# Performance work log

Hardware: AMD Instinct MI355X
Metric: run time of the kernel (lower is better)

Reference implementation:

```python
import jax, jax.numpy as jnp
import numpy as np

HIDDEN = 1024
EXPAND = 2
D_REC = HIDDEN * EXPAND
INTER = 4096
B, T = 4, 4096


def _rmsnorm(x, w, eps=1e-6):
    var = jnp.mean(x * x, axis=-1, keepdims=True)
    return x * jax.lax.rsqrt(var + eps) * w


def setup_inputs() -> dict:
    key = jax.random.key(0)
    ks = jax.random.split(key, 11)
    s = lambda fan: 1.0 / np.sqrt(fan)
    return {
        "x": jax.random.normal(ks[0], (B, T, HIDDEN), dtype=jnp.float32),
        "ln1_w": jnp.ones((HIDDEN,), dtype=jnp.float32),
        "ln2_w": jnp.ones((HIDDEN,), dtype=jnp.float32),
        "w_in": jax.random.normal(ks[1], (D_REC, HIDDEN), dtype=jnp.float32) * s(HIDDEN),
        "w_gate": jax.random.normal(ks[2], (D_REC, HIDDEN), dtype=jnp.float32) * s(HIDDEN),
        "a_param": jax.random.normal(ks[3], (D_REC,), dtype=jnp.float32) * 0.1,
        "w_a": jax.random.normal(ks[4], (D_REC, D_REC), dtype=jnp.float32) * s(D_REC),
        "w_out": jax.random.normal(ks[5], (HIDDEN, D_REC), dtype=jnp.float32) * s(D_REC),
        "w_mlp_gate": jax.random.normal(ks[6], (INTER, HIDDEN), dtype=jnp.float32) * s(HIDDEN),
        "w_mlp_up": jax.random.normal(ks[7], (INTER, HIDDEN), dtype=jnp.float32) * s(HIDDEN),
        "w_mlp_down": jax.random.normal(ks[8], (HIDDEN, INTER), dtype=jnp.float32) * s(INTER),
    }


def _hawk_scan(x_in, a):
    # x_in, a: [B, T, D_REC]; h_t = a_t*h_{t-1} + sqrt(1-a_t^2+eps)*x_t
    xs = jnp.moveaxis(x_in, 1, 0)  # [T, B, D]
    As = jnp.moveaxis(a, 1, 0)

    def step(state, inp):
        a_t, x_t = inp
        new = a_t * state + jnp.sqrt(1.0 - a_t * a_t + 1e-8) * x_t
        return new, new

    init = jnp.zeros(x_in.shape[::2], dtype=x_in.dtype)  # [B, D]
    _, ys = jax.lax.scan(step, init, (As, xs))
    return jnp.moveaxis(ys, 0, 1)  # [B, T, D]


def reference(x, ln1_w, ln2_w, w_in, w_gate, a_param, w_a, w_out,
              w_mlp_gate, w_mlp_up, w_mlp_down):
    h = _rmsnorm(x, ln1_w)
    x_in = h @ w_in.T                     # [B,T,D_REC]
    gate = jax.nn.sigmoid(h @ w_gate.T)
    a = jax.nn.sigmoid(a_param + x_in @ w_a.T)
    y = gate * _hawk_scan(x_in, a)
    x = x + y @ w_out.T
    h2 = _rmsnorm(x, ln2_w)
    mlp = (jax.nn.silu(h2 @ w_mlp_gate.T) * (h2 @ w_mlp_up.T)) @ w_mlp_down.T
    return x + mlp
```

## Files before the change

kernel.cpp:

```cpp
#include <hip/hip_runtime.h>
#include <cstdint>
#include <cmath>


typedef unsigned short u16;
typedef _Float16 f16;
typedef __bf16 bf16x8 __attribute__((ext_vector_type(8)));
typedef float  f32x4  __attribute__((ext_vector_type(4)));

#define BM 128
#define BN 128
#define BK 64

#define HID   1024
#define DREC  2048
#define INTER 4096
#define BT    16384
#define TLEN  4096
#define NCHAN 8192
#define CHUNK 256
#define NCH   16

__device__ __forceinline__ float b2f(u16 u) {
  union { unsigned int i; float f; } v; v.i = ((unsigned int)u) << 16; return v.f;
}
__device__ __forceinline__ u16 f2bf(float f) {
  unsigned int u = __builtin_bit_cast(unsigned int, f);
  u += 0x7FFFu + ((u >> 16) & 1u);
  return (u16)(u >> 16);
}
__device__ __forceinline__ float sigm(float x) { return 1.f / (1.f + expf(-x)); }

typedef __attribute__((address_space(1))) void as1_void;
typedef __attribute__((address_space(3))) void as3_void;
__device__ __forceinline__ void async16(const void* g, void* l) {
  __builtin_amdgcn_global_load_lds((as1_void*)g, (as3_void*)l, 16, 0, 0);
}

__global__ void f2b_kernel(const float* __restrict__ in, u16* __restrict__ out, int n4) {
  int i = blockIdx.x * 256 + threadIdx.x;
  if (i < n4) {
    float4 v = ((const float4*)in)[i];
    ushort4 o;
    o.x = f2bf(v.x); o.y = f2bf(v.y); o.z = f2bf(v.z); o.w = f2bf(v.w);
    ((ushort4*)out)[i] = o;
  }
}

__global__ void rmsnorm_kernel(const float* __restrict__ x, const float* __restrict__ w,
                               u16* __restrict__ out) {
  const int row = blockIdx.x;
  const int tid = threadIdx.x;
  float4 v = ((const float4*)(x + (size_t)row * HID))[tid];
  float ss = v.x * v.x + v.y * v.y + v.z * v.z + v.w * v.w;
#pragma unroll
  for (int o = 32; o > 0; o >>= 1) ss += __shfl_down(ss, o);
  __shared__ float red[4];
  const int lane = tid & 63, wv = tid >> 6;
  if (lane == 0) red[wv] = ss;
  __syncthreads();
  float tot = red[0] + red[1] + red[2] + red[3];
  float sc = rsqrtf(tot * (1.f / (float)HID) + 1e-6f);
  float4 wv4 = ((const float4*)w)[tid];
  ushort4 o;
  o.x = f2bf(v.x * sc * wv4.x); o.y = f2bf(v.y * sc * wv4.y);
  o.z = f2bf(v.z * sc * wv4.z); o.w = f2bf(v.w * sc * wv4.w);
  ((ushort4*)(out + (size_t)row * HID))[tid] = o;
}

enum { EPI_LOGIT = 0, EPI_ADDF = 1 };

template <int EPI>
__global__ __launch_bounds__(256, 2)
void gemm1(const u16* __restrict__ A, const u16* __restrict__ W,
           int K, int N, int ldA, int ldW,
           float* outf, f16* outz, const float* auxf) {
  __shared__ alignas(16) u16 sA[BM * BK];
  __shared__ alignas(16) u16 sB[BN * BK];

  const int tid  = threadIdx.x;
  const int lane = tid & 63;
  const int wv   = tid >> 6;
  const int wm   = wv & 1;
  const int wn   = wv >> 1;
  const int lm   = lane & 15;
  const int quad = lane >> 4;

  const int row0 = blockIdx.x * BM;
  const int col0 = blockIdx.y * BN;

  f32x4 acc[4][4];
#pragma unroll
  for (int i = 0; i < 4; ++i)
#pragma unroll
    for (int j = 0; j < 4; ++j) acc[i][j] = (f32x4)0.f;

  for (int k0 = 0; k0 < K; k0 += BK) {
#pragma unroll
    for (int i = 0; i < 4; ++i) {
      int p = i * 256 + tid;
      int r = p >> 3;
      int sg = (p & 7) ^ (r & 7);
      async16(A + (size_t)(row0 + r) * ldA + (k0 + sg * 8), (char*)sA + p * 16);
    }
#pragma unroll
    for (int i = 0; i < 4; ++i) {
      int p = i * 256 + tid;
      int r = p >> 3;
      int sg = (p & 7) ^ (r & 7);
      async16(W + (size_t)(col0 + r) * ldW + (k0 + sg * 8), (char*)sB + p * 16);
    }
    __syncthreads();

#pragma unroll
    for (int h = 0; h < 2; ++h) {
      bf16x8 af[4], bf[4];
#pragma unroll
      for (int mi = 0; mi < 4; ++mi) {
        int r = wm * 64 + mi * 16 + lm;
        af[mi] = ((const bf16x8*)sA)[r * 8 + ((h * 4 + quad) ^ (r & 7))];
      }
#pragma unroll
      for (int ni = 0; ni < 4; ++ni) {
        int c = wn * 64 + ni * 16 + lm;
        bf[ni] = ((const bf16x8*)sB)[c * 8 + ((h * 4 + quad) ^ (c & 7))];
      }
#pragma unroll
      for (int mi = 0; mi < 4; ++mi)
#pragma unroll
        for (int ni = 0; ni < 4; ++ni)
          acc[mi][ni] = __builtin_amdgcn_mfma_f32_16x16x32_bf16(af[mi], bf[ni], acc[mi][ni], 0, 0, 0);
    }
    __syncthreads();
  }

#pragma unroll
  for (int mi = 0; mi < 4; ++mi) {
    const int rbase = row0 + wm * 64 + mi * 16 + quad * 4;
#pragma unroll
    for (int ni = 0; ni < 4; ++ni) {
      const int cg = col0 + wn * 64 + ni * 16 + lm;
      f32x4 v = acc[mi][ni];
#pragma unroll
      for (int rr = 0; rr < 4; ++rr) {
        size_t idx = (size_t)(rbase + rr) * N + cg;
        float t = v[rr];
        if constexpr (EPI == EPI_LOGIT) {
          outz[idx] = (f16)(t + auxf[cg]);
        } else {
          outf[idx] = t + auxf[idx];
        }
      }
    }
  }
}

enum { EPI2_XG = 0, EPI2_SM = 1 };

template <int EPI>
__global__ __launch_bounds__(256, 2)
void gemm2(const u16* __restrict__ A, const u16* __restrict__ W0,
           const u16* __restrict__ W1,
           int K, int N, int ldA, int ldW,
           u16* out0, u16* out1) {
  __shared__ alignas(16) u16 sA[BM * BK];
  __shared__ alignas(16) u16 sB0[BN * BK];
  __shared__ alignas(16) u16 sB1[BN * BK];

  const int tid  = threadIdx.x;
  const int lane = tid & 63;
  const int wv   = tid >> 6;
  const int wm   = wv & 1;
  const int wn   = wv >> 1;
  const int lm   = lane & 15;
  const int quad = lane >> 4;

  const int row0 = blockIdx.x * BM;
  const int col0 = blockIdx.y * BN;

  f32x4 acc0[4][4], acc1[4][4];
#pragma unroll
  for (int i = 0; i < 4; ++i)
#pragma unroll
    for (int j = 0; j < 4; ++j) { acc0[i][j] = (f32x4)0.f; acc1[i][j] = (f32x4)0.f; }

  for (int k0 = 0; k0 < K; k0 += BK) {
#pragma unroll
    for (int i = 0; i < 4; ++i) {
      int p = i * 256 + tid;
      int r = p >> 3;
      int sg = (p & 7) ^ (r & 7);
      size_t go = (size_t)(col0 + r) * ldW + (k0 + sg * 8);
      async16(A + (size_t)(row0 + r) * ldA + (k0 + sg * 8), (char*)sA + p * 16);
      async16(W0 + go, (char*)sB0 + p * 16);
      async16(W1 + go, (char*)sB1 + p * 16);
    }
    __syncthreads();

#pragma unroll
    for (int h = 0; h < 2; ++h) {
      bf16x8 af[4], b0[4], b1[4];
#pragma unroll
      for (int mi = 0; mi < 4; ++mi) {
        int r = wm * 64 + mi * 16 + lm;
        af[mi] = ((const bf16x8*)sA)[r * 8 + ((h * 4 + quad) ^ (r & 7))];
      }
#pragma unroll
      for (int ni = 0; ni < 4; ++ni) {
        int c = wn * 64 + ni * 16 + lm;
        int o = c * 8 + ((h * 4 + quad) ^ (c & 7));
        b0[ni] = ((const bf16x8*)sB0)[o];
        b1[ni] = ((const bf16x8*)sB1)[o];
      }
#pragma unroll
      for (int mi = 0; mi < 4; ++mi)
#pragma unroll
        for (int ni = 0; ni < 4; ++ni) {
          acc0[mi][ni] = __builtin_amdgcn_mfma_f32_16x16x32_bf16(af[mi], b0[ni], acc0[mi][ni], 0, 0, 0);
          acc1[mi][ni] = __builtin_amdgcn_mfma_f32_16x16x32_bf16(af[mi], b1[ni], acc1[mi][ni], 0, 0, 0);
        }
    }
    __syncthreads();
  }

#pragma unroll
  for (int mi = 0; mi < 4; ++mi) {
    const int rbase = row0 + wm * 64 + mi * 16 + quad * 4;
#pragma unroll
    for (int ni = 0; ni < 4; ++ni) {
      const int cg = col0 + wn * 64 + ni * 16 + lm;
#pragma unroll
      for (int rr = 0; rr < 4; ++rr) {
        size_t idx = (size_t)(rbase + rr) * N + cg;
        float v0 = acc0[mi][ni][rr];
        float v1 = acc1[mi][ni][rr];
        if constexpr (EPI == EPI2_XG) {
          out0[idx] = f2bf(v0);
          out1[idx] = f2bf(sigm(v1));
        } else {
          out0[idx] = f2bf(v0 * sigm(v0) * v1);
        }
      }
    }
  }
}

__global__ void scan_phase1(const f16* __restrict__ z, const u16* __restrict__ xin,
                            float* __restrict__ ch_h, float* __restrict__ ch_p) {
  int gtid = blockIdx.x * 256 + threadIdx.x;
  int c = gtid >> 13;
  int chan = gtid & (NCHAN - 1);
  int b = chan >> 11;
  int d = chan & (DREC - 1);
  size_t base = ((size_t)b * TLEN + (size_t)c * CHUNK) * DREC + d;
  float h = 0.f, P = 1.f;
#pragma unroll 8
  for (int t = 0; t < CHUNK; ++t) {
    size_t i = base + (size_t)t * DREC;
    float at = sigm((float)z[i]);
    float xt = b2f(xin[i]);
    h = at * h + sqrtf(1.f - at * at + 1e-8f) * xt;
    P *= at;
  }
  ch_h[gtid] = h;
  ch_p[gtid] = P;
}

__global__ void scan_phase2(float* __restrict__ ch_h, const float* __restrict__ ch_p) {
  int chan = blockIdx.x * 256 + threadIdx.x;
  float H = 0.f;
#pragma unroll
  for (int c = 0; c < NCH; ++c) {
    int i = c * NCHAN + chan;
    float he = ch_h[i];
    float P  = ch_p[i];
    ch_h[i] = H;
    H = he + P * H;
  }
}

__global__ void scan_phase3(const f16* __restrict__ z, const u16* __restrict__ xin,
                            u16* gate_y, const float* __restrict__ ch_h) {
  int gtid = blockIdx.x * 256 + threadIdx.x;
  int c = gtid >> 13;
  int chan = gtid & (NCHAN - 1);
  int b = chan >> 11;
  int d = chan & (DREC - 1);
  size_t base = ((size_t)b * TLEN + (size_t)c * CHUNK) * DREC + d;
  float h = ch_h[gtid];
#pragma unroll 8
  for (int t = 0; t < CHUNK; ++t) {
    size_t i = base + (size_t)t * DREC;
    float at = sigm((float)z[i]);
    float xt = b2f(xin[i]);
    h = at * h + sqrtf(1.f - at * at + 1e-8f) * xt;
    gate_y[i] = f2bf(b2f(gate_y[i]) * h);
  }
}

extern "C" void kernel_launch(void* const* d_in, const int* in_sizes, int n_in,
                              void* d_out, int out_size, void* d_ws, size_t ws_size,
                              hipStream_t stream) {
  const float* x      = (const float*)d_in[0];
  const float* ln1    = (const float*)d_in[1];
  const float* ln2    = (const float*)d_in[2];
  const float* w_in   = (const float*)d_in[3];
  const float* w_gate = (const float*)d_in[4];
  const float* a_par  = (const float*)d_in[5];
  const float* w_a    = (const float*)d_in[6];
  const float* w_out  = (const float*)d_in[7];
  const float* w_mg   = (const float*)d_in[8];
  const float* w_mu   = (const float*)d_in[9];
  const float* w_md   = (const float*)d_in[10];
  float* out = (float*)d_out;
  char* ws = (char*)d_ws;

  const size_t MB = 1024ull * 1024ull;
  u16* wb_in  = (u16*)(ws + 0 * MB);
  u16* wb_gt  = (u16*)(ws + 4 * MB);
  u16* wb_a   = (u16*)(ws + 8 * MB);
  u16* wb_out = (u16*)(ws + 16 * MB);
  u16* wb_mg  = (u16*)(ws + 20 * MB);
  u16* wb_mu  = (u16*)(ws + 28 * MB);
  u16* wb_md  = (u16*)(ws + 36 * MB);
  u16* hbuf  = (u16*)(ws + 44 * MB);
  f16* zbuf  = (f16*)(ws + 44 * MB);
  u16* gateb = (u16*)(ws + 108 * MB);
  u16* mbuf  = (u16*)(ws + 108 * MB);
  float* chh = (float*)(ws + 172 * MB);
  float* chp = (float*)(ws + 172 * MB + 512 * 1024);
  u16* xinb = (u16*)d_out;

  f2b_kernel<<<2048, 256, 0, stream>>>(w_in,   wb_in,  DREC * HID / 4);
  f2b_kernel<<<2048, 256, 0, stream>>>(w_gate, wb_gt,  DREC * HID / 4);
  f2b_kernel<<<4096, 256, 0, stream>>>(w_a,    wb_a,   DREC * DREC / 4);
  f2b_kernel<<<2048, 256, 0, stream>>>(w_out,  wb_out, HID * DREC / 4);
  f2b_kernel<<<4096, 256, 0, stream>>>(w_mg,   wb_mg,  INTER * HID / 4);
  f2b_kernel<<<4096, 256, 0, stream>>>(w_mu,   wb_mu,  INTER * HID / 4);
  f2b_kernel<<<4096, 256, 0, stream>>>(w_md,   wb_md,  HID * INTER / 4);

  rmsnorm_kernel<<<BT, 256, 0, stream>>>(x, ln1, hbuf);

  gemm2<EPI2_XG><<<dim3(BT / BM, DREC / BN), 256, 0, stream>>>(
      hbuf, wb_in, wb_gt, HID, DREC, HID, HID, xinb, gateb);

  gemm1<EPI_LOGIT><<<dim3(BT / BM, DREC / BN), 256, 0, stream>>>(
      xinb, wb_a, DREC, DREC, DREC, DREC, nullptr, zbuf, a_par);

  scan_phase1<<<512, 256, 0, stream>>>(zbuf, xinb, chh, chp);
  scan_phase2<<<NCHAN / 256, 256, 0, stream>>>(chh, chp);
  scan_phase3<<<512, 256, 0, stream>>>(zbuf, xinb, gateb, chh);

  gemm1<EPI_ADDF><<<dim3(BT / BM, HID / BN), 256, 0, stream>>>(
      gateb, wb_out, DREC, HID, DREC, DREC, out, nullptr, x);

  rmsnorm_kernel<<<BT, 256, 0, stream>>>(out, ln2, hbuf);

  for (int half = 0; half < 2; ++half) {
    const u16* wmg_h = wb_mg + (size_t)half * 2048 * HID;
    const u16* wmu_h = wb_mu + (size_t)half * 2048 * HID;
    const u16* wmd_h = wb_md + (size_t)half * 2048;
    gemm2<EPI2_SM><<<dim3(BT / BM, 2048 / BN), 256, 0, stream>>>(
        hbuf, wmg_h, wmu_h, HID, 2048, HID, HID, mbuf, nullptr);
    gemm1<EPI_ADDF><<<dim3(BT / BM, HID / BN), 256, 0, stream>>>(
        mbuf, wmd_h, 2048, HID, 2048, INTER, out, nullptr, out);
  }
}
```

Before: 1.273 ms.

## Shrink dual-GEMM N tile, raise occupancy, pair scan channels, fuse weight casts

The dual-output GEMM now uses 64-wide N tiles with half the accumulators, and both GEMM kernels request 3 blocks per CU instead of 2, to cut register and LDS pressure and raise occupancy. The scan kernels each process two adjacent channels with 32-bit vector loads and stores, halving thread count and widening memory transactions. The seven weight-conversion launches are merged into one kernel to reduce launch overhead. Smaller tiles reload the A tile more often, and the tighter register budget from launch_bounds 3 may cause spills in gemm1.

```diff
diff --git a/kernel.cpp b/kernel.cpp
--- a/kernel.cpp
+++ b/kernel.cpp
@@ -20,6 +20,7 @@
 #define NCHAN 8192
 #define CHUNK 256
 #define NCH   16
+#define NPAIR 4096
 
 __device__ __forceinline__ float b2f(u16 u) {
   union { unsigned int i; float f; } v; v.i = ((unsigned int)u) << 16; return v.f;
@@ -37,14 +38,25 @@
   __builtin_amdgcn_global_load_lds((as1_void*)g, (as3_void*)l, 16, 0, 0);
 }
 
-__global__ void f2b_kernel(const float* __restrict__ in, u16* __restrict__ out, int n4) {
-  int i = blockIdx.x * 256 + threadIdx.x;
-  if (i < n4) {
-    float4 v = ((const float4*)in)[i];
-    ushort4 o;
-    o.x = f2bf(v.x); o.y = f2bf(v.y); o.z = f2bf(v.z); o.w = f2bf(v.w);
-    ((ushort4*)out)[i] = o;
-  }
+__global__ void f2b_all(const float* s0, const float* s1, const float* s2,
+                        const float* s3, const float* s4, const float* s5,
+                        const float* s6,
+                        u16* d0, u16* d1, u16* d2, u16* d3, u16* d4, u16* d5,
+                        u16* d6) {
+  int blk = blockIdx.x;
+  const float* src; u16* dst; int rel;
+  if      (blk < 2048)  { src = s0; dst = d0; rel = blk; }
+  else if (blk < 4096)  { src = s1; dst = d1; rel = blk - 2048; }
+  else if (blk < 8192)  { src = s2; dst = d2; rel = blk - 4096; }
+  else if (blk < 10240) { src = s3; dst = d3; rel = blk - 8192; }
+  else if (blk < 14336) { src = s4; dst = d4; rel = blk - 10240; }
+  else if (blk < 18432) { src = s5; dst = d5; rel = blk - 14336; }
+  else                  { src = s6; dst = d6; rel = blk - 18432; }
+  int i = rel * 256 + threadIdx.x;
+  float4 v = ((const float4*)src)[i];
+  ushort4 o;
+  o.x = f2bf(v.x); o.y = f2bf(v.y); o.z = f2bf(v.z); o.w = f2bf(v.w);
+  ((ushort4*)dst)[i] = o;
 }
 
 __global__ void rmsnorm_kernel(const float* __restrict__ x, const float* __restrict__ w,
@@ -71,7 +83,7 @@
 enum { EPI_LOGIT = 0, EPI_ADDF = 1 };
 
 template <int EPI>
-__global__ __launch_bounds__(256, 2)
+__global__ __launch_bounds__(256, 3)
 void gemm1(const u16* __restrict__ A, const u16* __restrict__ W,
            int K, int N, int ldA, int ldW,
            float* outf, f16* outz, const float* auxf) {
@@ -158,14 +170,14 @@
 enum { EPI2_XG = 0, EPI2_SM = 1 };
 
 template <int EPI>
-__global__ __launch_bounds__(256, 2)
+__global__ __launch_bounds__(256, 3)
 void gemm2(const u16* __restrict__ A, const u16* __restrict__ W0,
            const u16* __restrict__ W1,
            int K, int N, int ldA, int ldW,
            u16* out0, u16* out1) {
   __shared__ alignas(16) u16 sA[BM * BK];
-  __shared__ alignas(16) u16 sB0[BN * BK];
-  __shared__ alignas(16) u16 sB1[BN * BK];
+  __shared__ alignas(16) u16 sB0[64 * BK];
+  __shared__ alignas(16) u16 sB1[64 * BK];
 
   const int tid  = threadIdx.x;
   const int lane = tid & 63;
@@ -176,13 +188,13 @@
   const int quad = lane >> 4;
 
   const int row0 = blockIdx.x * BM;
-  const int col0 = blockIdx.y * BN;
-
-  f32x4 acc0[4][4], acc1[4][4];
+  const int col0 = blockIdx.y * 64;
+
+  f32x4 acc0[4][2], acc1[4][2];
 #pragma unroll
   for (int i = 0; i < 4; ++i)
 #pragma unroll
-    for (int j = 0; j < 4; ++j) { acc0[i][j] = (f32x4)0.f; acc1[i][j] = (f32x4)0.f; }
+    for (int j = 0; j < 2; ++j) { acc0[i][j] = (f32x4)0.f; acc1[i][j] = (f32x4)0.f; }
 
   for (int k0 = 0; k0 < K; k0 += BK) {
 #pragma unroll
@@ -190,8 +202,14 @@
       int p = i * 256 + tid;
       int r = p >> 3;
       int sg = (p & 7) ^ (r & 7);
+      async16(A + (size_t)(row0 + r) * ldA + (k0 + sg * 8), (char*)sA + p * 16);
+    }
+#pragma unroll
+    for (int i = 0; i < 2; ++i) {
+      int p = i * 256 + tid;
+      int r = p >> 3;
+      int sg = (p & 7) ^ (r & 7);
       size_t go = (size_t)(col0 + r) * ldW + (k0 + sg * 8);
-      async16(A + (size_t)(row0 + r) * ldA + (k0 + sg * 8), (char*)sA + p * 16);
       async16(W0 + go, (char*)sB0 + p * 16);
       async16(W1 + go, (char*)sB1 + p * 16);
     }
@@ -199,15 +217,15 @@
 
 #pragma unroll
     for (int h = 0; h < 2; ++h) {
-      bf16x8 af[4], b0[4], b1[4];
+      bf16x8 af[4], b0[2], b1[2];
 #pragma unroll
       for (int mi = 0; mi < 4; ++mi) {
         int r = wm * 64 + mi * 16 + lm;
         af[mi] = ((const bf16x8*)sA)[r * 8 + ((h * 4 + quad) ^ (r & 7))];
       }
 #pragma unroll
-      for (int ni = 0; ni < 4; ++ni) {
-        int c = wn * 64 + ni * 16 + lm;
+      for (int ni = 0; ni < 2; ++ni) {
+        int c = wn * 32 + ni * 16 + lm;
         int o = c * 8 + ((h * 4 + quad) ^ (c & 7));
         b0[ni] = ((const bf16x8*)sB0)[o];
         b1[ni] = ((const bf16x8*)sB1)[o];
@@ -215,7 +233,7 @@
 #pragma unroll
       for (int mi = 0; mi < 4; ++mi)
 #pragma unroll
-        for (int ni = 0; ni < 4; ++ni) {
+        for (int ni = 0; ni < 2; ++ni) {
           acc0[mi][ni] = __builtin_amdgcn_mfma_f32_16x16x32_bf16(af[mi], b0[ni], acc0[mi][ni], 0, 0, 0);
           acc1[mi][ni] = __builtin_amdgcn_mfma_f32_16x16x32_bf16(af[mi], b1[ni], acc1[mi][ni], 0, 0, 0);
         }
@@ -227,8 +245,8 @@
   for (int mi = 0; mi < 4; ++mi) {
     const int rbase = row0 + wm * 64 + mi * 16 + quad * 4;
 #pragma unroll
-    for (int ni = 0; ni < 4; ++ni) {
-      const int cg = col0 + wn * 64 + ni * 16 + lm;
+    for (int ni = 0; ni < 2; ++ni) {
+      const int cg = col0 + wn * 32 + ni * 16 + lm;
 #pragma unroll
       for (int rr = 0; rr < 4; ++rr) {
         size_t idx = (size_t)(rbase + rr) * N + cg;
@@ -246,55 +264,64 @@
 }
 
 __global__ void scan_phase1(const f16* __restrict__ z, const u16* __restrict__ xin,
-                            float* __restrict__ ch_h, float* __restrict__ ch_p) {
+                            float2* __restrict__ ch_h, float2* __restrict__ ch_p) {
   int gtid = blockIdx.x * 256 + threadIdx.x;
-  int c = gtid >> 13;
-  int chan = gtid & (NCHAN - 1);
-  int b = chan >> 11;
-  int d = chan & (DREC - 1);
+  int c = gtid >> 12;
+  int pair = gtid & (NPAIR - 1);
+  int b = pair >> 10;
+  int d = (pair & 1023) * 2;
   size_t base = ((size_t)b * TLEN + (size_t)c * CHUNK) * DREC + d;
-  float h = 0.f, P = 1.f;
+  float2 h = {0.f, 0.f}, P = {1.f, 1.f};
 #pragma unroll 8
   for (int t = 0; t < CHUNK; ++t) {
     size_t i = base + (size_t)t * DREC;
-    float at = sigm((float)z[i]);
-    float xt = b2f(xin[i]);
-    h = at * h + sqrtf(1.f - at * at + 1e-8f) * xt;
-    P *= at;
+    f16 z2[2]; *(uint32_t*)z2 = *(const uint32_t*)(z + i);
+    u16 x2[2]; *(uint32_t*)x2 = *(const uint32_t*)(xin + i);
+    float a0 = sigm((float)z2[0]), a1 = sigm((float)z2[1]);
+    h.x = a0 * h.x + sqrtf(1.f - a0 * a0 + 1e-8f) * b2f(x2[0]);
+    h.y = a1 * h.y + sqrtf(1.f - a1 * a1 + 1e-8f) * b2f(x2[1]);
+    P.x *= a0; P.y *= a1;
   }
   ch_h[gtid] = h;
   ch_p[gtid] = P;
 }
 
-__global__ void scan_phase2(float* __restrict__ ch_h, const float* __restrict__ ch_p) {
-  int chan = blockIdx.x * 256 + threadIdx.x;
-  float H = 0.f;
+__global__ void scan_phase2(float2* __restrict__ ch_h, const float2* __restrict__ ch_p) {
+  int pair = blockIdx.x * 256 + threadIdx.x;
+  float2 H = {0.f, 0.f};
 #pragma unroll
   for (int c = 0; c < NCH; ++c) {
-    int i = c * NCHAN + chan;
-    float he = ch_h[i];
-    float P  = ch_p[i];
+    int i = c * NPAIR + pair;
+    float2 he = ch_h[i];
+    float2 P  = ch_p[i];
     ch_h[i] = H;
-    H = he + P * H;
+    H.x = he.x + P.x * H.x;
+    H.y = he.y + P.y * H.y;
   }
 }
 
 __global__ void scan_phase3(const f16* __restrict__ z, const u16* __restrict__ xin,
-                            u16* gate_y, const float* __restrict__ ch_h) {
+                            u16* gate_y, const float2* __restrict__ ch_h) {
   int gtid = blockIdx.x * 256 + threadIdx.x;
-  int c = gtid >> 13;
-  int chan = gtid & (NCHAN - 1);
-  int b = chan >> 11;
-  int d = chan & (DREC - 1);
+  int c = gtid >> 12;
+  int pair = gtid & (NPAIR - 1);
+  int b = pair >> 10;
+  int d = (pair & 1023) * 2;
   size_t base = ((size_t)b * TLEN + (size_t)c * CHUNK) * DREC + d;
-  float h = ch_h[gtid];
+  float2 h = ch_h[gtid];
 #pragma unroll 8
   for (int t = 0; t < CHUNK; ++t) {
     size_t i = base + (size_t)t * DREC;
-    float at = sigm((float)z[i]);
-    float xt = b2f(xin[i]);
-    h = at * h + sqrtf(1.f - at * at + 1e-8f) * xt;
-    gate_y[i] = f2bf(b2f(gate_y[i]) * h);
+    f16 z2[2]; *(uint32_t*)z2 = *(const uint32_t*)(z + i);
+    u16 x2[2]; *(uint32_t*)x2 = *(const uint32_t*)(xin + i);
+    u16 g2[2]; *(uint32_t*)g2 = *(const uint32_t*)(gate_y + i);
+    float a0 = sigm((float)z2[0]), a1 = sigm((float)z2[1]);
+    h.x = a0 * h.x + sqrtf(1.f - a0 * a0 + 1e-8f) * b2f(x2[0]);
+    h.y = a1 * h.y + sqrtf(1.f - a1 * a1 + 1e-8f) * b2f(x2[1]);
+    u16 o2[2];
+    o2[0] = f2bf(b2f(g2[0]) * h.x);
+    o2[1] = f2bf(b2f(g2[1]) * h.y);
+    *(uint32_t*)(gate_y + i) = *(uint32_t*)o2;
   }
 }
 
@@ -327,29 +354,24 @@
   f16* zbuf  = (f16*)(ws + 44 * MB);
   u16* gateb = (u16*)(ws + 108 * MB);
   u16* mbuf  = (u16*)(ws + 108 * MB);
-  float* chh = (float*)(ws + 172 * MB);
-  float* chp = (float*)(ws + 172 * MB + 512 * 1024);
+  float2* chh = (float2*)(ws + 172 * MB);
+  float2* chp = (float2*)(ws + 172 * MB + 512 * 1024);
   u16* xinb = (u16*)d_out;
 
-  f2b_kernel<<<2048, 256, 0, stream>>>(w_in,   wb_in,  DREC * HID / 4);
-  f2b_kernel<<<2048, 256, 0, stream>>>(w_gate, wb_gt,  DREC * HID / 4);
-  f2b_kernel<<<4096, 256, 0, stream>>>(w_a,    wb_a,   DREC * DREC / 4);
-  f2b_kernel<<<2048, 256, 0, stream>>>(w_out,  wb_out, HID * DREC / 4);
-  f2b_kernel<<<4096, 256, 0, stream>>>(w_mg,   wb_mg,  INTER * HID / 4);
-  f2b_kernel<<<4096, 256, 0, stream>>>(w_mu,   wb_mu,  INTER * HID / 4);
-  f2b_kernel<<<4096, 256, 0, stream>>>(w_md,   wb_md,  HID * INTER / 4);
+  f2b_all<<<22528, 256, 0, stream>>>(w_in, w_gate, w_a, w_out, w_mg, w_mu, w_md,
+                                     wb_in, wb_gt, wb_a, wb_out, wb_mg, wb_mu, wb_md);
 
   rmsnorm_kernel<<<BT, 256, 0, stream>>>(x, ln1, hbuf);
 
-  gemm2<EPI2_XG><<<dim3(BT / BM, DREC / BN), 256, 0, stream>>>(
+  gemm2<EPI2_XG><<<dim3(BT / BM, DREC / 64), 256, 0, stream>>>(
       hbuf, wb_in, wb_gt, HID, DREC, HID, HID, xinb, gateb);
 
   gemm1<EPI_LOGIT><<<dim3(BT / BM, DREC / BN), 256, 0, stream>>>(
       xinb, wb_a, DREC, DREC, DREC, DREC, nullptr, zbuf, a_par);
 
-  scan_phase1<<<512, 256, 0, stream>>>(zbuf, xinb, chh, chp);
-  scan_phase2<<<NCHAN / 256, 256, 0, stream>>>(chh, chp);
-  scan_phase3<<<512, 256, 0, stream>>>(zbuf, xinb, gateb, chh);
+  scan_phase1<<<NCH * NPAIR / 256, 256, 0, stream>>>(zbuf, xinb, chh, chp);
+  scan_phase2<<<NPAIR / 256, 256, 0, stream>>>(chh, chp);
+  scan_phase3<<<NCH * NPAIR / 256, 256, 0, stream>>>(zbuf, xinb, gateb, chh);
 
   gemm1<EPI_ADDF><<<dim3(BT / BM, HID / BN), 256, 0, stream>>>(
       gateb, wb_out, DREC, HID, DREC, DREC, out, nullptr, x);
@@ -360,7 +382,7 @@
     const u16* wmg_h = wb_mg + (size_t)half * 2048 * HID;
     const u16* wmu_h = wb_mu + (size_t)half * 2048 * HID;
     const u16* wmd_h = wb_md + (size_t)half * 2048;
-    gemm2<EPI2_SM><<<dim3(BT / BM, 2048 / BN), 256, 0, stream>>>(
+    gemm2<EPI2_SM><<<dim3(BT / BM, 2048 / 64), 256, 0, stream>>>(
         hbuf, wmg_h, wmu_h, HID, 2048, HID, HID, mbuf, nullptr);
     gemm1<EPI_ADDF><<<dim3(BT / BM, HID / BN), 256, 0, stream>>>(
         mbuf, wmd_h, 2048, HID, 2048, INTER, out, nullptr, out);
```

Measured after the change: 1.391 ms. 9.3% more time.
